# Performance work log

Measured on AMD Instinct MI355X. Metric: run time of the kernel, lower is better.

The kernel has to match this reference:

```python
import jax, jax.numpy as jnp
import numpy as np

B, S, D_MODEL, D_K = 4, 4096, 1024, 64


def setup_inputs() -> dict:
    key = jax.random.key(0)
    ks = jax.random.split(key, 4)
    scale = 1.0 / np.sqrt(D_MODEL)
    x = jax.random.normal(ks[0], (B, S, D_MODEL), dtype=jnp.float32)
    Wq = jax.random.normal(ks[1], (D_MODEL, D_K), dtype=jnp.float32) * scale
    Wk = jax.random.normal(ks[2], (D_MODEL, D_K), dtype=jnp.float32) * scale
    Wv = jax.random.normal(ks[3], (D_MODEL, D_K), dtype=jnp.float32) * scale
    bq = jnp.zeros((D_K,), dtype=jnp.float32)
    bk = jnp.zeros((D_K,), dtype=jnp.float32)
    bv = jnp.zeros((D_K,), dtype=jnp.float32)
    # causal mask: 1 = keep, 0 = masked (matches docstring semantics)
    mask = jnp.broadcast_to(
        jnp.tril(jnp.ones((S, S), dtype=jnp.int32))[None], (B, S, S)
    )
    return {"x": x, "mask": mask, "Wq": Wq, "bq": bq, "Wk": Wk, "bk": bk, "Wv": Wv, "bv": bv}


def reference(x, mask, Wq, bq, Wk, bk, Wv, bv):
    # Q/K/V projections: (B, S, d_model) @ (d_model, d_k) -> (B, S, d_k)
    Q = jnp.einsum("bsd,dk->bsk", x, Wq) + bq
    K = jnp.einsum("bsd,dk->bsk", x, Wk) + bk
    V = jnp.einsum("bsd,dk->bsk", x, Wv) + bv
    # scaled dot-product scores: (B, S, S)
    scores = jnp.einsum("bqk,bsk->bqs", Q, K) / jnp.sqrt(jnp.float32(D_K))
    scores = jnp.where(mask == 0, jnp.float32(-jnp.inf), scores)
    attn = jax.nn.softmax(scores, axis=-1)
    # dropout with p_drop = 0.0 is identity
    out = jnp.einsum("bqs,bsk->bqk", attn, V)  # (B, S, d_k)
    return out
```

## Files before the change

kernel.cpp:

```cpp
#include <hip/hip_runtime.h>
#include <hip/hip_bf16.h>


typedef float  f32x4  __attribute__((ext_vector_type(4)));
typedef float  f32x16 __attribute__((ext_vector_type(16)));
typedef short  s16x8  __attribute__((ext_vector_type(8)));
typedef short  s16x4  __attribute__((ext_vector_type(4)));

#define MFMA16(A, B, C) __builtin_amdgcn_mfma_f32_16x16x32_bf16((A), (B), (C), 0, 0, 0)
#define MFMA32(A, B, C) __builtin_amdgcn_mfma_f32_32x32x16_bf16((A), (B), (C), 0, 0, 0)

static __device__ __forceinline__ ushort f2bf(float f) {
    union { float f; unsigned u; } v; v.f = f;
    unsigned u = v.u;
    unsigned r = (u + 0x7FFFu + ((u >> 16) & 1u)) >> 16;
    return (ushort)r;
}

static __device__ __forceinline__ f32x4 fzero() {
    f32x4 v; v[0] = v[1] = v[2] = v[3] = 0.f; return v;
}

__global__ __launch_bounds__(256) void prep_w(const float* __restrict__ Wq,
                                              const float* __restrict__ Wk,
                                              const float* __restrict__ Wv,
                                              short* __restrict__ Wt) {
    const int blk = blockIdx.x;
    const int mat = blk >> 4, kt = blk & 15;
    const float* src = mat == 0 ? Wq : (mat == 1 ? Wk : Wv);
    const float sc = (mat == 0) ? 0.125f : 1.0f;
    __shared__ float wsm[64][68];
    const int t = threadIdx.x;

    const int rb = t >> 4, c4 = (t & 15) * 4;
    #pragma unroll
    for (int i = 0; i < 4; ++i) {
        f32x4 v = *(const f32x4*)&src[(size_t)(kt * 64 + rb + 16 * i) * 64 + c4];
        *(f32x4*)&wsm[rb + 16 * i][c4] = v;
    }
    __syncthreads();

    const int c = t >> 2, ks = (t & 3) * 16;
    s16x8 o0, o1;
    #pragma unroll
    for (int j = 0; j < 8; ++j) o0[j] = (short)f2bf(wsm[ks + j][c] * sc);
    #pragma unroll
    for (int j = 0; j < 8; ++j) o1[j] = (short)f2bf(wsm[ks + 8 + j][c] * sc);
    const size_t ob = (size_t)(mat * 64 + c) * 1024 + kt * 64 + ks;
    *(s16x8*)&Wt[ob]     = o0;
    *(s16x8*)&Wt[ob + 8] = o1;
}

__global__ __launch_bounds__(256) void proj(const float* __restrict__ x,
                                            const short* __restrict__ Wt,
                                            const float* __restrict__ bq,
                                            const float* __restrict__ bk,
                                            const float* __restrict__ bv,
                                            short* __restrict__ Qb,
                                            short* __restrict__ Kb,
                                            short* __restrict__ Vt) {
    const int tid  = threadIdx.x;
    const int lane = tid & 63;
    const int w    = tid >> 6;
    const int m0   = blockIdx.x * 32;
    const int l15  = lane & 15, gr = lane >> 4;

    __shared__ short xs[2][32][140];

    const int srow = tid >> 3;
    const int sc8  = tid & 7;
    const float* sbase = x + (size_t)(m0 + srow) * 1024 + 4 * sc8;

    f32x4 acc[3][2];
    #pragma unroll
    for (int m = 0; m < 3; ++m)
        for (int n = 0; n < 2; ++n) acc[m][n] = fzero();

    const short* aptr = Wt + (size_t)(48 * w + l15) * 1024 + 8 * gr;

    f32x4 ld[4];
    #pragma unroll
    for (int i = 0; i < 4; ++i) ld[i] = *(const f32x4*)(sbase + 32 * i);
    #pragma unroll
    for (int i = 0; i < 4; ++i) {
        s16x4 o;
        #pragma unroll
        for (int j = 0; j < 4; ++j) o[j] = (short)f2bf(ld[i][j]);
        *(s16x4*)&xs[0][srow][4 * sc8 + 32 * i] = o;
    }

    s16x8 a_cur[3], a_nxt[3];
    #pragma unroll
    for (int m = 0; m < 3; ++m) a_cur[m] = *(const s16x8*)(aptr + (size_t)m * 16 * 1024);
    __syncthreads();

    for (int c = 0; c < 8; ++c) {
        const int buf = c & 1;
        if (c < 7) {
            #pragma unroll
            for (int i = 0; i < 4; ++i) ld[i] = *(const f32x4*)(sbase + 128 * (c + 1) + 32 * i);
        }
        #pragma unroll
        for (int f = 0; f < 4; ++f) {
            const int ko = 128 * c + 32 * f;
            const int kn = (ko + 32) & 1023;
            #pragma unroll
            for (int m = 0; m < 3; ++m) a_nxt[m] = *(const s16x8*)(aptr + (size_t)m * 16 * 1024 + kn);
            s16x8 b[2];
            #pragma unroll
            for (int n = 0; n < 2; ++n) b[n] = *(const s16x8*)&xs[buf][16 * n + l15][32 * f + 8 * gr];
            #pragma unroll
            for (int m = 0; m < 3; ++m)
                for (int n = 0; n < 2; ++n) acc[m][n] = MFMA16(a_cur[m], b[n], acc[m][n]);
            #pragma unroll
            for (int m = 0; m < 3; ++m) a_cur[m] = a_nxt[m];
        }
        if (c < 7) {
            #pragma unroll
            for (int i = 0; i < 4; ++i) {
                s16x4 o;
                #pragma unroll
                for (int j = 0; j < 4; ++j) o[j] = (short)f2bf(ld[i][j]);
                *(s16x4*)&xs[buf ^ 1][srow][4 * sc8 + 32 * i] = o;
            }
        }
        __syncthreads();
    }

    #pragma unroll
    for (int m = 0; m < 3; ++m) {
        const int c0 = 48 * w + 16 * m + 4 * gr;
        #pragma unroll
        for (int n = 0; n < 2; ++n) {
            const int row = m0 + 16 * n + l15;
            f32x4 v = acc[m][n];
            if (c0 < 64) {
                s16x4 o;
                #pragma unroll
                for (int r = 0; r < 4; ++r) o[r] = (short)f2bf(v[r] + 0.125f * bq[c0 + r]);
                *(s16x4*)&Qb[(size_t)row * 64 + c0] = o;
            } else if (c0 < 128) {
                s16x4 o;
                #pragma unroll
                for (int r = 0; r < 4; ++r) o[r] = (short)f2bf(v[r] + bk[c0 - 64 + r]);
                *(s16x4*)&Kb[(size_t)row * 64 + (c0 - 64)] = o;
            } else {
                const int b = row >> 12, s = row & 4095;
                #pragma unroll
                for (int r = 0; r < 4; ++r)
                    Vt[((size_t)b * 64 + (c0 - 128 + r)) * 4096 + s] =
                        (short)f2bf(v[r] + bv[c0 - 128 + r]);
            }
        }
    }
}

__global__ __launch_bounds__(256, 2) void attn(const short* __restrict__ Qb,
                                               const short* __restrict__ Kb,
                                               const short* __restrict__ Vt,
                                               float* __restrict__ out) {
    const int bid   = blockIdx.x;
    const int xcd   = bid & 7, bi = bid >> 3;
    const int batch = xcd >> 1;
    const int g     = 127 - 2 * bi - (xcd & 1);
    const int q0    = g * 32;
    const int tid   = threadIdx.x, lane = tid & 63, w = tid >> 6;
    const int l31   = lane & 31, h = lane >> 5, kb = 4 * h;

    __shared__ float Om[4][32][68];
    __shared__ float Mm[4][32], Lm[4][32];

    const size_t row0 = (size_t)batch * 4096;

    const short* Qp = Qb + (row0 + q0 + l31) * 64 + 8 * h;
    s16x8 qf[4];
    #pragma unroll
    for (int kk = 0; kk < 4; ++kk) qf[kk] = *(const s16x8*)(Qp + 16 * kk);

    f32x16 oT0, oT1;
    #pragma unroll
    for (int r = 0; r < 16; ++r) { oT0[r] = 0.f; oT1[r] = 0.f; }
    float m = -1e30f, l_ = 0.f;

    const int nt = g + 1;
    const int t0 = (nt * w) >> 2, t1 = (nt * (w + 1)) >> 2;

    const short* Kp = Kb + (row0 + l31) * 64 + 8 * h;
    const short* Vp = Vt + ((size_t)batch * 64 + l31) * 4096 + 8 * h;

    s16x8 kf[4], va[2][2], kf2[4], va2[2][2];
    if (t0 < t1) {
        const int j0 = t0 * 32;
        #pragma unroll
        for (int kk = 0; kk < 4; ++kk) kf[kk] = *(const s16x8*)(Kp + (size_t)j0 * 64 + 16 * kk);
        #pragma unroll
        for (int dt = 0; dt < 2; ++dt)
            #pragma unroll
            for (int kk = 0; kk < 2; ++kk)
                va[dt][kk] = *(const s16x8*)(Vp + (size_t)dt * 32 * 4096 + j0 + 16 * kk);
    }

    for (int t = t0; t < t1; ++t) {
        const int j0 = t * 32;
        if (t + 1 < t1) {
            const int jn = j0 + 32;
            #pragma unroll
            for (int kk = 0; kk < 4; ++kk) kf2[kk] = *(const s16x8*)(Kp + (size_t)jn * 64 + 16 * kk);
            #pragma unroll
            for (int dt = 0; dt < 2; ++dt)
                #pragma unroll
                for (int kk = 0; kk < 2; ++kk)
                    va2[dt][kk] = *(const s16x8*)(Vp + (size_t)dt * 32 * 4096 + jn + 16 * kk);
        }

        f32x16 sacc;
        #pragma unroll
        for (int r = 0; r < 16; ++r) sacc[r] = 0.f;
        #pragma unroll
        for (int kk = 0; kk < 4; ++kk) sacc = MFMA32(kf[kk], qf[kk], sacc);

        if (j0 == q0) {
            #pragma unroll
            for (int r = 0; r < 16; ++r) {
                const int kvloc = (r & 3) + 8 * (r >> 2) + kb;
                if (kvloc > l31) sacc[r] = -1e30f;
            }
        }

        float tm[8];
        #pragma unroll
        for (int r = 0; r < 8; ++r) tm[r] = fmaxf(sacc[r], sacc[r + 8]);
        #pragma unroll
        for (int r = 0; r < 4; ++r) tm[r] = fmaxf(tm[r], tm[r + 4]);
        tm[0] = fmaxf(fmaxf(tm[0], tm[2]), fmaxf(tm[1], tm[3]));
        float sm = fmaxf(tm[0], __shfl_xor(tm[0], 32));

        if (!__all(sm - m <= 8.f)) {
            const float mn = fmaxf(m, sm);
            const float sc = __expf(m - mn);
            m = mn;
            l_ *= sc;
            #pragma unroll
            for (int r = 0; r < 16; ++r) { oT0[r] *= sc; oT1[r] *= sc; }
        }

        float p[16];
        #pragma unroll
        for (int r = 0; r < 16; ++r) p[r] = __expf(sacc[r] - m);
        float ts[8];
        #pragma unroll
        for (int r = 0; r < 8; ++r) ts[r] = p[r] + p[r + 8];
        #pragma unroll
        for (int r = 0; r < 4; ++r) ts[r] = ts[r] + ts[r + 4];
        const float ls = (ts[0] + ts[2]) + (ts[1] + ts[3]);
        l_ += ls + __shfl_xor(ls, 32);

        unsigned pw[8];
        #pragma unroll
        for (int i = 0; i < 8; ++i)
            asm("v_cvt_pk_bf16_f32 %0, %1, %2" : "=v"(pw[i]) : "v"(p[2 * i]), "v"(p[2 * i + 1]));
        asm volatile("v_permlane32_swap_b32 %0, %1" : "+v"(pw[0]), "+v"(pw[2]));
        asm volatile("v_permlane32_swap_b32 %0, %1" : "+v"(pw[1]), "+v"(pw[3]));
        asm volatile("v_permlane32_swap_b32 %0, %1" : "+v"(pw[4]), "+v"(pw[6]));
        asm volatile("v_permlane32_swap_b32 %0, %1" : "+v"(pw[5]), "+v"(pw[7]));
        union { unsigned u[4]; s16x8 v; } f0, f1;
        f0.u[0] = pw[0]; f0.u[1] = pw[1]; f0.u[2] = pw[2]; f0.u[3] = pw[3];
        f1.u[0] = pw[4]; f1.u[1] = pw[5]; f1.u[2] = pw[6]; f1.u[3] = pw[7];

        oT0 = MFMA32(va[0][0], f0.v, oT0);
        oT0 = MFMA32(va[0][1], f1.v, oT0);
        oT1 = MFMA32(va[1][0], f0.v, oT1);
        oT1 = MFMA32(va[1][1], f1.v, oT1);

        #pragma unroll
        for (int kk = 0; kk < 4; ++kk) kf[kk] = kf2[kk];
        #pragma unroll
        for (int dt = 0; dt < 2; ++dt)
            #pragma unroll
            for (int kk = 0; kk < 2; ++kk) va[dt][kk] = va2[dt][kk];
    }

    #pragma unroll
    for (int rg = 0; rg < 4; ++rg) {
        f32x4 v0, v1;
        #pragma unroll
        for (int j = 0; j < 4; ++j) { v0[j] = oT0[4 * rg + j]; v1[j] = oT1[4 * rg + j]; }
        const int d0 = rg * 8 + kb;
        *(f32x4*)&Om[w][l31][d0]      = v0;
        *(f32x4*)&Om[w][l31][32 + d0] = v1;
    }
    if (lane < 32) { Mm[w][l31] = m; Lm[w][l31] = l_; }
    __syncthreads();

    {
        const int q = tid >> 3, d0 = (tid & 7) * 8;
        const float m0 = Mm[0][q], m1 = Mm[1][q], m2 = Mm[2][q], m3 = Mm[3][q];
        const float mt = fmaxf(fmaxf(m0, m1), fmaxf(m2, m3));
        float sw[4];
        sw[0] = __expf(m0 - mt); sw[1] = __expf(m1 - mt);
        sw[2] = __expf(m2 - mt); sw[3] = __expf(m3 - mt);
        const float lt = sw[0] * Lm[0][q] + sw[1] * Lm[1][q] + sw[2] * Lm[2][q] + sw[3] * Lm[3][q];
        const float inv = 1.f / lt;
        f32x4 a0 = fzero(), a1 = fzero();
        #pragma unroll
        for (int ww = 0; ww < 4; ++ww) {
            f32x4 u0 = *(const f32x4*)&Om[ww][q][d0];
            f32x4 u1 = *(const f32x4*)&Om[ww][q][d0 + 4];
            #pragma unroll
            for (int j = 0; j < 4; ++j) { a0[j] += sw[ww] * u0[j]; a1[j] += sw[ww] * u1[j]; }
        }
        const size_t ob = (row0 + q0 + q) * 64 + d0;
        f32x4 r0, r1;
        #pragma unroll
        for (int j = 0; j < 4; ++j) { r0[j] = a0[j] * inv; r1[j] = a1[j] * inv; }
        *(f32x4*)&out[ob]     = r0;
        *(f32x4*)&out[ob + 4] = r1;
    }
}

extern "C" void kernel_launch(void* const* d_in, const int* in_sizes, int n_in,
                              void* d_out, int out_size, void* d_ws, size_t ws_size,
                              hipStream_t stream) {
    const float* x  = (const float*)d_in[0];
    const float* Wq = (const float*)d_in[2];
    const float* bq = (const float*)d_in[3];
    const float* Wk = (const float*)d_in[4];
    const float* bk = (const float*)d_in[5];
    const float* Wv = (const float*)d_in[6];
    const float* bv = (const float*)d_in[7];
    float* out = (float*)d_out;

    char* ws = (char*)d_ws;
    short* Wt = (short*)(ws);
    short* Qb = (short*)(ws + 393216);
    short* Kb = (short*)(ws + 2490368);
    short* Vt = (short*)(ws + 4587520);

    prep_w<<<dim3(48), dim3(256), 0, stream>>>(Wq, Wk, Wv, Wt);
    proj<<<dim3(512), dim3(256), 0, stream>>>(x, Wt, bq, bk, bv, Qb, Kb, Vt);
    attn<<<dim3(512), dim3(256), 0, stream>>>(Qb, Kb, Vt, out);
}
```

Before: 85.31 us.

## Stage K/V tiles via async global-to-LDS loads and shrink projection tiles

```diff
diff --git a/kernel.cpp b/kernel.cpp
--- a/kernel.cpp
+++ b/kernel.cpp
@@ -9,6 +9,11 @@
 
 #define MFMA16(A, B, C) __builtin_amdgcn_mfma_f32_16x16x32_bf16((A), (B), (C), 0, 0, 0)
 #define MFMA32(A, B, C) __builtin_amdgcn_mfma_f32_32x32x16_bf16((A), (B), (C), 0, 0, 0)
+
+#define GLL16(SRC, DST)                                                              \
+    __builtin_amdgcn_global_load_lds(                                                \
+        (const __attribute__((address_space(1))) unsigned*)(SRC),                    \
+        (__attribute__((address_space(3))) unsigned*)(DST), 16, 0, 0)
 
 static __device__ __forceinline__ ushort f2bf(float f) {
     union { float f; unsigned u; } v; v.f = f;
@@ -51,42 +56,41 @@
     *(s16x8*)&Wt[ob + 8] = o1;
 }
 
-__global__ __launch_bounds__(256) void proj(const float* __restrict__ x,
-                                            const short* __restrict__ Wt,
-                                            const float* __restrict__ bq,
-                                            const float* __restrict__ bk,
-                                            const float* __restrict__ bv,
-                                            short* __restrict__ Qb,
-                                            short* __restrict__ Kb,
-                                            short* __restrict__ Vt) {
+__global__ __launch_bounds__(256, 4) void proj(const float* __restrict__ x,
+                                               const short* __restrict__ Wt,
+                                               const float* __restrict__ bq,
+                                               const float* __restrict__ bk,
+                                               const float* __restrict__ bv,
+                                               short* __restrict__ Qb,
+                                               short* __restrict__ Kb,
+                                               short* __restrict__ Vt) {
     const int tid  = threadIdx.x;
     const int lane = tid & 63;
     const int w    = tid >> 6;
-    const int m0   = blockIdx.x * 32;
+    const int m0   = blockIdx.x * 16;
     const int l15  = lane & 15, gr = lane >> 4;
 
-    __shared__ short xs[2][32][140];
-
-    const int srow = tid >> 3;
-    const int sc8  = tid & 7;
-    const float* sbase = x + (size_t)(m0 + srow) * 1024 + 4 * sc8;
-
-    f32x4 acc[3][2];
-    #pragma unroll
-    for (int m = 0; m < 3; ++m)
-        for (int n = 0; n < 2; ++n) acc[m][n] = fzero();
+    __shared__ short xs[2][16][136];
+
+    const int srow = tid >> 4;
+    const int sc16 = (tid & 15) * 4;
+    const float* sbase = x + (size_t)(m0 + srow) * 1024 + sc16;
+
+    f32x4 acc[3];
+    #pragma unroll
+    for (int m = 0; m < 3; ++m) acc[m] = fzero();
 
     const short* aptr = Wt + (size_t)(48 * w + l15) * 1024 + 8 * gr;
 
-    f32x4 ld[4];
-    #pragma unroll
-    for (int i = 0; i < 4; ++i) ld[i] = *(const f32x4*)(sbase + 32 * i);
-    #pragma unroll
-    for (int i = 0; i < 4; ++i) {
+    f32x4 ld[2];
+    ld[0] = *(const f32x4*)(sbase);
+    ld[1] = *(const f32x4*)(sbase + 64);
+    #pragma unroll
+    for (int i = 0; i < 2; ++i) {
         s16x4 o;
         #pragma unroll
         for (int j = 0; j < 4; ++j) o[j] = (short)f2bf(ld[i][j]);
-        *(s16x4*)&xs[0][srow][4 * sc8 + 32 * i] = o;
+        *(s16x4*)&xs[0][srow][sc16 + 64 * i] = o;
     }
 
     s16x8 a_cur[3], a_nxt[3];
@@ -97,8 +101,8 @@
     for (int c = 0; c < 8; ++c) {
         const int buf = c & 1;
         if (c < 7) {
-            #pragma unroll
-            for (int i = 0; i < 4; ++i) ld[i] = *(const f32x4*)(sbase + 128 * (c + 1) + 32 * i);
+            ld[0] = *(const f32x4*)(sbase + 128 * (c + 1));
+            ld[1] = *(const f32x4*)(sbase + 128 * (c + 1) + 64);
         }
         #pragma unroll
         for (int f = 0; f < 4; ++f) {
@@ -106,22 +110,19 @@
             const int kn = (ko + 32) & 1023;
             #pragma unroll
             for (int m = 0; m < 3; ++m) a_nxt[m] = *(const s16x8*)(aptr + (size_t)m * 16 * 1024 + kn);
-            s16x8 b[2];
-            #pragma unroll
-            for (int n = 0; n < 2; ++n) b[n] = *(const s16x8*)&xs[buf][16 * n + l15][32 * f + 8 * gr];
-            #pragma unroll
-            for (int m = 0; m < 3; ++m)
-                for (int n = 0; n < 2; ++n) acc[m][n] = MFMA16(a_cur[m], b[n], acc[m][n]);
+            s16x8 b = *(const s16x8*)&xs[buf][l15][32 * f + 8 * gr];
+            #pragma unroll
+            for (int m = 0; m < 3; ++m) acc[m] = MFMA16(a_cur[m], b, acc[m]);
             #pragma unroll
             for (int m = 0; m < 3; ++m) a_cur[m] = a_nxt[m];
         }
         if (c < 7) {
             #pragma unroll
-            for (int i = 0; i < 4; ++i) {
+            for (int i = 0; i < 2; ++i) {
                 s16x4 o;
                 #pragma unroll
                 for (int j = 0; j < 4; ++j) o[j] = (short)f2bf(ld[i][j]);
-                *(s16x4*)&xs[buf ^ 1][srow][4 * sc8 + 32 * i] = o;
+                *(s16x4*)&xs[buf ^ 1][srow][sc16 + 64 * i] = o;
             }
         }
         __syncthreads();
@@ -130,32 +131,29 @@
     #pragma unroll
     for (int m = 0; m < 3; ++m) {
         const int c0 = 48 * w + 16 * m + 4 * gr;
-        #pragma unroll
-        for (int n = 0; n < 2; ++n) {
-            const int row = m0 + 16 * n + l15;
-            f32x4 v = acc[m][n];
-            if (c0 < 64) {
-                s16x4 o;
-                #pragma unroll
-                for (int r = 0; r < 4; ++r) o[r] = (short)f2bf(v[r] + 0.125f * bq[c0 + r]);
-                *(s16x4*)&Qb[(size_t)row * 64 + c0] = o;
-            } else if (c0 < 128) {
-                s16x4 o;
-                #pragma unroll
-                for (int r = 0; r < 4; ++r) o[r] = (short)f2bf(v[r] + bk[c0 - 64 + r]);
-                *(s16x4*)&Kb[(size_t)row * 64 + (c0 - 64)] = o;
-            } else {
-                const int b = row >> 12, s = row & 4095;
-                #pragma unroll
-                for (int r = 0; r < 4; ++r)
-                    Vt[((size_t)b * 64 + (c0 - 128 + r)) * 4096 + s] =
-                        (short)f2bf(v[r] + bv[c0 - 128 + r]);
-            }
-        }
-    }
-}
-
-__global__ __launch_bounds__(256, 2) void attn(const short* __restrict__ Qb,
+        const int row = m0 + l15;
+        f32x4 v = acc[m];
+        if (c0 < 64) {
+            s16x4 o;
+            #pragma unroll
+            for (int r = 0; r < 4; ++r) o[r] = (short)f2bf(v[r] + 0.125f * bq[c0 + r]);
+            *(s16x4*)&Qb[(size_t)row * 64 + c0] = o;
+        } else if (c0 < 128) {
+            s16x4 o;
+            #pragma unroll
+            for (int r = 0; r < 4; ++r) o[r] = (short)f2bf(v[r] + bk[c0 - 64 + r]);
+            *(s16x4*)&Kb[(size_t)row * 64 + (c0 - 64)] = o;
+        } else {
+            const int b = row >> 12, s = row & 4095;
+            #pragma unroll
+            for (int r = 0; r < 4; ++r)
+                Vt[((size_t)b * 64 + (c0 - 128 + r)) * 4096 + s] =
+                    (short)f2bf(v[r] + bv[c0 - 128 + r]);
+        }
+    }
+}
+
+__global__ __launch_bounds__(256, 3) void attn(const short* __restrict__ Qb,
                                                const short* __restrict__ Kb,
                                                const short* __restrict__ Vt,
                                                float* __restrict__ out) {
@@ -167,10 +165,17 @@
     const int tid   = threadIdx.x, lane = tid & 63, w = tid >> 6;
     const int l31   = lane & 31, h = lane >> 5, kb = 4 * h;
 
-    __shared__ float Om[4][32][68];
+    __shared__ __align__(16) char smem[32768];
     __shared__ float Mm[4][32], Lm[4][32];
 
+    short* lds_k = (short*)(smem + w * 8192);
+    short* lds_v = (short*)(smem + w * 8192 + 4096);
+    auto kdst = (__attribute__((address_space(3))) char*)smem + w * 8192;
+    auto vdst = kdst + 4096;
+
     const size_t row0 = (size_t)batch * 4096;
+    const short* Kb2 = Kb + row0 * 64;
+    const short* Vb2 = Vt + (size_t)batch * 64 * 4096;
 
     const short* Qp = Qb + (row0 + q0 + l31) * 64 + 8 * h;
     s16x8 qf[4];
@@ -185,33 +190,43 @@
     const int nt = g + 1;
     const int t0 = (nt * w) >> 2, t1 = (nt * (w + 1)) >> 2;
 
-    const short* Kp = Kb + (row0 + l31) * 64 + 8 * h;
-    const short* Vp = Vt + ((size_t)batch * 64 + l31) * 4096 + 8 * h;
-
-    s16x8 kf[4], va[2][2], kf2[4], va2[2][2];
-    if (t0 < t1) {
-        const int j0 = t0 * 32;
-        #pragma unroll
-        for (int kk = 0; kk < 4; ++kk) kf[kk] = *(const s16x8*)(Kp + (size_t)j0 * 64 + 16 * kk);
-        #pragma unroll
-        for (int dt = 0; dt < 2; ++dt)
-            #pragma unroll
-            for (int kk = 0; kk < 2; ++kk)
-                va[dt][kk] = *(const s16x8*)(Vp + (size_t)dt * 32 * 4096 + j0 + 16 * kk);
-    }
+    auto stage = [&](int j0) {
+        #pragma unroll
+        for (int i = 0; i < 4; ++i) {
+            const int s  = 8 * i + (lane >> 3);
+            const int cs = ((lane & 7) ^ (s & 7)) * 8;
+            GLL16(Kb2 + (size_t)(j0 + s) * 64 + cs, kdst + i * 1024);
+        }
+        #pragma unroll
+        for (int i = 0; i < 4; ++i) {
+            const int d  = 16 * i + (lane >> 2);
+            const int cs = ((lane & 3) ^ (d & 3)) * 8;
+            GLL16(Vb2 + (size_t)d * 4096 + j0 + cs, vdst + i * 1024);
+        }
+    };
+
+    if (t0 < t1) stage(t0 * 32);
 
     for (int t = t0; t < t1; ++t) {
         const int j0 = t * 32;
-        if (t + 1 < t1) {
-            const int jn = j0 + 32;
-            #pragma unroll
-            for (int kk = 0; kk < 4; ++kk) kf2[kk] = *(const s16x8*)(Kp + (size_t)jn * 64 + 16 * kk);
-            #pragma unroll
-            for (int dt = 0; dt < 2; ++dt)
-                #pragma unroll
-                for (int kk = 0; kk < 2; ++kk)
-                    va2[dt][kk] = *(const s16x8*)(Vp + (size_t)dt * 32 * 4096 + jn + 16 * kk);
-        }
+
+        asm volatile("s_waitcnt vmcnt(0)" ::: "memory");
+        __builtin_amdgcn_sched_barrier(0);
+
+        s16x8 kf[4], va[2][2];
+        #pragma unroll
+        for (int kk = 0; kk < 4; ++kk)
+            kf[kk] = *(const s16x8*)(lds_k + l31 * 64 + (((2 * kk + h) ^ (l31 & 7)) * 8));
+        #pragma unroll
+        for (int dt = 0; dt < 2; ++dt)
+            #pragma unroll
+            for (int kk = 0; kk < 2; ++kk)
+                va[dt][kk] = *(const s16x8*)(lds_v + (32 * dt + l31) * 32 +
+                                             (((2 * kk + h) ^ (l31 & 3)) * 8));
+
+        asm volatile("s_waitcnt lgkmcnt(0)" ::: "memory");
+        __builtin_amdgcn_sched_barrier(0);
+        if (t + 1 < t1) stage(j0 + 32);
 
         f32x16 sacc;
         #pragma unroll
@@ -244,12 +259,11 @@
             for (int r = 0; r < 16; ++r) { oT0[r] *= sc; oT1[r] *= sc; }
         }
 
-        float p[16];
-        #pragma unroll
-        for (int r = 0; r < 16; ++r) p[r] = __expf(sacc[r] - m);
+        #pragma unroll
+        for (int r = 0; r < 16; ++r) sacc[r] = __expf(sacc[r] - m);
         float ts[8];
         #pragma unroll
-        for (int r = 0; r < 8; ++r) ts[r] = p[r] + p[r + 8];
+        for (int r = 0; r < 8; ++r) ts[r] = sacc[r] + sacc[r + 8];
         #pragma unroll
         for (int r = 0; r < 4; ++r) ts[r] = ts[r] + ts[r + 4];
         const float ls = (ts[0] + ts[2]) + (ts[1] + ts[3]);
@@ -258,7 +272,8 @@
         unsigned pw[8];
         #pragma unroll
         for (int i = 0; i < 8; ++i)
-            asm("v_cvt_pk_bf16_f32 %0, %1, %2" : "=v"(pw[i]) : "v"(p[2 * i]), "v"(p[2 * i + 1]));
+            asm("v_cvt_pk_bf16_f32 %0, %1, %2"
+                : "=v"(pw[i]) : "v"(sacc[2 * i]), "v"(sacc[2 * i + 1]));
         asm volatile("v_permlane32_swap_b32 %0, %1" : "+v"(pw[0]), "+v"(pw[2]));
         asm volatile("v_permlane32_swap_b32 %0, %1" : "+v"(pw[1]), "+v"(pw[3]));
         asm volatile("v_permlane32_swap_b32 %0, %1" : "+v"(pw[4]), "+v"(pw[6]));
@@ -271,23 +286,20 @@
         oT0 = MFMA32(va[0][1], f1.v, oT0);
         oT1 = MFMA32(va[1][0], f0.v, oT1);
         oT1 = MFMA32(va[1][1], f1.v, oT1);
-
-        #pragma unroll
-        for (int kk = 0; kk < 4; ++kk) kf[kk] = kf2[kk];
-        #pragma unroll
-        for (int dt = 0; dt < 2; ++dt)
-            #pragma unroll
-            for (int kk = 0; kk < 2; ++kk) va[dt][kk] = va2[dt][kk];
-    }
-
+    }
+
+    asm volatile("s_waitcnt vmcnt(0)" ::: "memory");
+    __builtin_amdgcn_sched_barrier(0);
+
+    float* Om_w = (float*)(smem + w * 8192);
     #pragma unroll
     for (int rg = 0; rg < 4; ++rg) {
         f32x4 v0, v1;
         #pragma unroll
         for (int j = 0; j < 4; ++j) { v0[j] = oT0[4 * rg + j]; v1[j] = oT1[4 * rg + j]; }
         const int d0 = rg * 8 + kb;
-        *(f32x4*)&Om[w][l31][d0]      = v0;
-        *(f32x4*)&Om[w][l31][32 + d0] = v1;
+        *(f32x4*)&Om_w[l31 * 64 + d0]      = v0;
+        *(f32x4*)&Om_w[l31 * 64 + 32 + d0] = v1;
     }
     if (lane < 32) { Mm[w][l31] = m; Lm[w][l31] = l_; }
     __syncthreads();
@@ -304,8 +316,9 @@
         f32x4 a0 = fzero(), a1 = fzero();
         #pragma unroll
         for (int ww = 0; ww < 4; ++ww) {
-            f32x4 u0 = *(const f32x4*)&Om[ww][q][d0];
-            f32x4 u1 = *(const f32x4*)&Om[ww][q][d0 + 4];
+            const float* Om_r = (const float*)(smem + ww * 8192);
+            f32x4 u0 = *(const f32x4*)&Om_r[q * 64 + d0];
+            f32x4 u1 = *(const f32x4*)&Om_r[q * 64 + d0 + 4];
             #pragma unroll
             for (int j = 0; j < 4; ++j) { a0[j] += sw[ww] * u0[j]; a1[j] += sw[ww] * u1[j]; }
         }
@@ -336,7 +349,7 @@
     short* Kb = (short*)(ws + 2490368);
     short* Vt = (short*)(ws + 4587520);
 
-    prep_w<<<dim3(48), dim3(256), 0, stream>>>(Wq, Wk, Wv, Wt);
-    proj<<<dim3(512), dim3(256), 0, stream>>>(x, Wt, bq, bk, bv, Qb, Kb, Vt);
-    attn<<<dim3(512), dim3(256), 0, stream>>>(Qb, Kb, Vt, out);
-}
+    prep_w<<<dim3(48),   dim3(256), 0, stream>>>(Wq, Wk, Wv, Wt);
+    proj<<<dim3(1024),   dim3(256), 0, stream>>>(x, Wt, bq, bk, bv, Qb, Kb, Vt);
+    attn<<<dim3(512),    dim3(256), 0, stream>>>(Qb, Kb, Vt, out);
+}
```

New measurement: 87.50 us. +2.6%, slower.
